# Kernel tuning notes

Hardware: AMD Instinct MI355X
Metric: run time of the kernel (lower is better)

The kernel has to match this reference:

```python
import jax, jax.numpy as jnp
import numpy as np

B, D, L, H = 256, 512, 64, 300


def setup_inputs() -> dict:
    key = jax.random.key(0)
    ks = jax.random.split(key, 16)
    s = 0.05  # weight init scale to keep activations sane through ReLU chains
    return {
        "x": jax.random.normal(ks[0], (B, D), jnp.float32),
        "eps": jax.random.normal(ks[1], (B, L), jnp.float32),
        "W": jax.random.normal(ks[2], (D, L), jnp.float32) * s,
        "enc1_w": jax.random.normal(ks[3], (H, D), jnp.float32) * s,
        "enc1_b": jax.random.normal(ks[4], (H,), jnp.float32) * s,
        "enc2_w": jax.random.normal(ks[5], (H, H), jnp.float32) * s,
        "enc2_b": jax.random.normal(ks[6], (H,), jnp.float32) * s,
        "zm_w": jax.random.normal(ks[7], (L, H), jnp.float32) * s,
        "zm_b": jax.random.normal(ks[8], (L,), jnp.float32) * s,
        "zv_w": jax.random.normal(ks[9], (L, H), jnp.float32) * s,
        "zv_b": jax.random.normal(ks[10], (L,), jnp.float32) * s,
        "gen1_w": jax.random.normal(ks[11], (H, L), jnp.float32) * s,
        "gen2_w": jax.random.normal(ks[12], (H, H), jnp.float32) * s,
        "gen2_b": jax.random.normal(ks[13], (H,), jnp.float32) * s,
        "head_w": jax.random.normal(ks[14], (D, H), jnp.float32) * s,
        "head_b": jax.random.normal(ks[15], (D,), jnp.float32) * s,
    }


def reference(x, eps, W, enc1_w, enc1_b, enc2_w, enc2_b, zm_w, zm_b,
              zv_w, zv_b, gen1_w, gen2_w, gen2_b, head_w, head_b):
    # encode: q_z = ReLU(Linear) -> ReLU(Linear)
    h = jax.nn.relu(x @ enc1_w.T + enc1_b)
    h = jax.nn.relu(h @ enc2_w.T + enc2_b)
    z_mean = h @ zm_w.T + zm_b          # [B, L]
    z_log_var = h @ zv_w.T + zv_b       # [B, L]
    # reparameterize (eps passed in for determinism)
    z = z_mean + eps * jnp.exp(0.5 * z_log_var)
    # decode: per-column masked z through shared generator + per-column head,
    # vectorized over the column axis D (mask = W rows)
    masked = z[:, None, :] * W[None, :, :]                       # [B, D, L]
    g1 = jax.nn.relu(jnp.einsum('bdl,hl->bdh', masked, gen1_w))  # [B, D, H]
    g2 = jax.nn.relu(jnp.einsum('bdh,gh->bdg', g1, gen2_w) + gen2_b)
    x_mean = jnp.einsum('bdh,dh->bd', g2, head_w) + head_b       # [B, D]
    return (x_mean, z, z_mean, z_log_var)
```

## Files before the change

### kernel.cpp

```cpp
#include <hip/hip_runtime.h>

typedef unsigned short u16;
typedef unsigned int u32;

typedef __bf16 bf16x8 __attribute__((ext_vector_type(8)));
typedef float f32x4 __attribute__((ext_vector_type(4)));

union V16 { uint4 u; bf16x8 v; u16 s[8]; __bf16 h[8]; };
union F4  { float4 v; float f[4]; };

__device__ __forceinline__ float bf2f(u16 a) {
  union { u32 u; float f; } c; c.u = ((u32)a) << 16; return c.f;
}

#define Z_OFF   131072
#define ZM_OFF  147456
#define ZLV_OFF 163840

#define B1_OFF 0
#define B2_OFF 2560
#define E1_OFF 15360
#define E2_OFF 35840
#define ZMP_OFF 48640
#define ZVP_OFF 51200
#define FRAG_TOTAL 53760
#define WB4  53760
#define XB4  57856
#define H1_4 74240
#define H2_4 84480
#define PACK_THREADS (FRAG_TOTAL + 4096 + 16384)

__device__ __forceinline__ void pack_one(const float* __restrict__ src,
                                         int t, int s, int lane,
                                         int Nsrc, int Ksrc, int rowlen,
                                         uint4* __restrict__ dst) {
  const int n = t * 16 + (lane & 15);
  const int k0 = s * 32 + ((lane >> 4) << 3);
  V16 v;
#pragma unroll
  for (int j = 0; j < 8; ++j) {
    const int k = k0 + j;
    v.h[j] = (n < Nsrc && k < Ksrc) ? (__bf16)src[n * rowlen + k] : (__bf16)0.f;
  }
  *dst = v.u;
}

__device__ __forceinline__ void cvt8(const float* __restrict__ src, uint4* __restrict__ dst) {
  F4 a, b; a.v = *(const float4*)src; b.v = *(const float4*)(src + 4);
  V16 v;
#pragma unroll
  for (int j = 0; j < 4; ++j) { v.h[j] = (__bf16)a.f[j]; v.h[4 + j] = (__bf16)b.f[j]; }
  *dst = v.u;
}

__global__ __launch_bounds__(256) void pack_kernel(
    const float* __restrict__ g1w, const float* __restrict__ g2w,
    const float* __restrict__ e1w, const float* __restrict__ e2w,
    const float* __restrict__ zmw, const float* __restrict__ zvw,
    const float* __restrict__ W,   const float* __restrict__ x,
    uint4* __restrict__ ws4) {
  const int idx = blockIdx.x * 256 + threadIdx.x;
  if (idx >= PACK_THREADS) return;
  const int lane = idx & 63;
  if (idx < B2_OFF) {
    const int f = (idx - B1_OFF) >> 6;
    pack_one(g1w, f >> 1, f & 1, lane, 300, 64, 64, ws4 + idx);
  } else if (idx < E1_OFF) {
    const int f = (idx - B2_OFF) >> 6;
    pack_one(g2w, f / 10, f % 10, lane, 300, 300, 300, ws4 + idx);
  } else if (idx < E2_OFF) {
    const int f = (idx - E1_OFF) >> 6;
    pack_one(e1w, f >> 4, f & 15, lane, 300, 512, 512, ws4 + idx);
  } else if (idx < ZMP_OFF) {
    const int f = (idx - E2_OFF) >> 6;
    pack_one(e2w, f / 10, f % 10, lane, 300, 300, 300, ws4 + idx);
  } else if (idx < ZVP_OFF) {
    const int f = (idx - ZMP_OFF) >> 6;
    pack_one(zmw, f / 10, f % 10, lane, 64, 300, 300, ws4 + idx);
  } else if (idx < FRAG_TOTAL) {
    const int f = (idx - ZVP_OFF) >> 6;
    pack_one(zvw, f / 10, f % 10, lane, 64, 300, 300, ws4 + idx);
  } else if (idx < FRAG_TOTAL + 4096) {
    const int i = idx - FRAG_TOTAL;
    cvt8(W + i * 8, ws4 + WB4 + i);
  } else {
    const int i = idx - FRAG_TOTAL - 4096;
    cvt8(x + i * 8, ws4 + XB4 + i);
  }
}

__global__ __launch_bounds__(64) void enc1_kernel(
    const uint4* __restrict__ xb, const uint4* __restrict__ e1p,
    const float* __restrict__ e1b, u16* __restrict__ h1) {
  const int wg = blockIdx.x;
  const int rt = wg / 20, nt = wg % 20;
  const int lane = threadIdx.x, q = lane >> 4, c = lane & 15;
  f32x4 acc = {0.f, 0.f, 0.f, 0.f};
  const int arow = rt * 16 + c;
#pragma unroll
  for (int s = 0; s < 16; ++s) {
    V16 a, b;
    a.u = xb[arow * 64 + s * 4 + q];
    b.u = e1p[(nt * 16 + s) * 64 + lane];
    acc = __builtin_amdgcn_mfma_f32_16x16x32_bf16(a.v, b.v, acc, 0, 0, 0);
  }
  const int col = nt * 16 + c;
  const float bias = (col < 300) ? e1b[col] : 0.f;
#pragma unroll
  for (int i = 0; i < 4; ++i) {
    const int row = rt * 16 + 4 * q + i;
    V16 t; t.h[0] = (col < 300) ? (__bf16)fmaxf(acc[i] + bias, 0.f) : (__bf16)0.f;
    h1[row * 320 + col] = t.s[0];
  }
}

__global__ __launch_bounds__(64) void enc2_kernel(
    const uint4* __restrict__ h1, const uint4* __restrict__ e2p,
    const float* __restrict__ e2b, u16* __restrict__ h2) {
  const int wg = blockIdx.x;
  const int rt = wg / 20, nt = wg % 20;
  const int lane = threadIdx.x, q = lane >> 4, c = lane & 15;
  f32x4 acc = {0.f, 0.f, 0.f, 0.f};
  const int arow = rt * 16 + c;
#pragma unroll
  for (int s = 0; s < 10; ++s) {
    V16 a, b;
    a.u = h1[arow * 40 + s * 4 + q];
    b.u = e2p[(nt * 10 + s) * 64 + lane];
    acc = __builtin_amdgcn_mfma_f32_16x16x32_bf16(a.v, b.v, acc, 0, 0, 0);
  }
  const int col = nt * 16 + c;
  const float bias = (col < 300) ? e2b[col] : 0.f;
#pragma unroll
  for (int i = 0; i < 4; ++i) {
    const int row = rt * 16 + 4 * q + i;
    V16 t; t.h[0] = (col < 300) ? (__bf16)fmaxf(acc[i] + bias, 0.f) : (__bf16)0.f;
    h2[row * 320 + col] = t.s[0];
  }
}

__global__ __launch_bounds__(64) void ench_kernel(
    const uint4* __restrict__ h2, const float* __restrict__ eps,
    const uint4* __restrict__ zmp, const float* __restrict__ zmb,
    const uint4* __restrict__ zvp, const float* __restrict__ zvb,
    float* __restrict__ out) {
  const int wg = blockIdx.x;
  const int rt = wg >> 2, t = wg & 3;
  const int lane = threadIdx.x, q = lane >> 4, c = lane & 15;
  f32x4 am = {0.f, 0.f, 0.f, 0.f}, av = {0.f, 0.f, 0.f, 0.f};
  const int arow = rt * 16 + c;
#pragma unroll
  for (int s = 0; s < 10; ++s) {
    V16 a, bm, bv;
    a.u = h2[arow * 40 + s * 4 + q];
    bm.u = zmp[(t * 10 + s) * 64 + lane];
    bv.u = zvp[(t * 10 + s) * 64 + lane];
    am = __builtin_amdgcn_mfma_f32_16x16x32_bf16(a.v, bm.v, am, 0, 0, 0);
    av = __builtin_amdgcn_mfma_f32_16x16x32_bf16(a.v, bv.v, av, 0, 0, 0);
  }
  const int col = t * 16 + c;
  const float bm = zmb[col], bv = zvb[col];
#pragma unroll
  for (int i = 0; i < 4; ++i) {
    const int gi = (rt * 16 + 4 * q + i) * 64 + col;
    const float zm = am[i] + bm;
    const float zlv = av[i] + bv;
    out[ZM_OFF + gi] = zm;
    out[ZLV_OFF + gi] = zlv;
    out[Z_OFF + gi] = zm + eps[gi] * expf(0.5f * zlv);
  }
}

__global__ __launch_bounds__(320, 4) void dec_kernel(
    const float* __restrict__ z,
    const uint4* __restrict__ Wb,
    const uint4* __restrict__ b1p,
    const uint4* __restrict__ b2p,
    const float* __restrict__ g2b,
    const float* __restrict__ hw,
    const float* __restrict__ hb,
    float* __restrict__ xout) {
  __shared__ u16 g1s[32 * 328];
  float* xredf = (float*)g1s;

  const int wg = blockIdx.x;
  const int r0 = wg << 5;
  const int bi = wg >> 4;
  const int d0 = r0 & 511;
  const int tid = threadIdx.x;
  const int u = tid >> 6;
  const int lane = tid & 63;
  const int q = lane >> 4;
  const int c = lane & 15;

  const float* zrow = z + bi * 64;

  bf16x8 bz[4][2];
#pragma unroll
  for (int kf = 0; kf < 2; ++kf) {
    F4 z0, z1;
    z0.v = *(const float4*)(zrow + kf * 32 + q * 8);
    z1.v = *(const float4*)(zrow + kf * 32 + q * 8 + 4);
#pragma unroll
    for (int tt = 0; tt < 4; ++tt) {
      V16 r; r.u = b1p[((4 * u + tt) * 2 + kf) * 64 + lane];
      V16 m;
#pragma unroll
      for (int j = 0; j < 4; ++j) {
        m.h[j]     = (__bf16)(bf2f(r.s[j])     * z0.f[j]);
        m.h[4 + j] = (__bf16)(bf2f(r.s[4 + j]) * z1.f[j]);
      }
      bz[tt][kf] = m.v;
    }
  }
#pragma unroll
  for (int rt = 0; rt < 2; ++rt) {
    const int rowA = rt * 16 + c;
    V16 af0, af1;
    af0.u = Wb[(d0 + rowA) * 8 + q];
    af1.u = Wb[(d0 + rowA) * 8 + 4 + q];
    f32x4 acc[4];
#pragma unroll
    for (int tt = 0; tt < 4; ++tt) acc[tt] = {0.f, 0.f, 0.f, 0.f};
#pragma unroll
    for (int tt = 0; tt < 4; ++tt) {
      acc[tt] = __builtin_amdgcn_mfma_f32_16x16x32_bf16(af0.v, bz[tt][0], acc[tt], 0, 0, 0);
      acc[tt] = __builtin_amdgcn_mfma_f32_16x16x32_bf16(af1.v, bz[tt][1], acc[tt], 0, 0, 0);
    }
    const int rwb = rt * 16 + 4 * q;
#pragma unroll
    for (int tt = 0; tt < 4; ++tt) {
      const int colb = (4 * u + tt) * 16 + c;
#pragma unroll
      for (int i = 0; i < 4; ++i) {
        V16 t; t.h[0] = (__bf16)fmaxf(acc[tt][i], 0.f);
        g1s[(rwb + i) * 328 + colb] = t.s[0];
      }
    }
  }
  __syncthreads();

  f32x4 a3[4][2];
#pragma unroll
  for (int tt = 0; tt < 4; ++tt)
#pragma unroll
    for (int rt = 0; rt < 2; ++rt) a3[tt][rt] = {0.f, 0.f, 0.f, 0.f};
  for (int s = 0; s < 10; ++s) {
    V16 b[4];
#pragma unroll
    for (int tt = 0; tt < 4; ++tt) b[tt].u = b2p[((4 * u + tt) * 10 + s) * 64 + lane];
#pragma unroll
    for (int rt = 0; rt < 2; ++rt) {
      V16 a; a.u = *(const uint4*)&g1s[(rt * 16 + c) * 328 + s * 32 + q * 8];
#pragma unroll
      for (int tt = 0; tt < 4; ++tt)
        a3[tt][rt] = __builtin_amdgcn_mfma_f32_16x16x32_bf16(a.v, b[tt].v, a3[tt][rt], 0, 0, 0);
    }
  }
  float xacc[2][4];
#pragma unroll
  for (int rt = 0; rt < 2; ++rt)
#pragma unroll
    for (int i = 0; i < 4; ++i) xacc[rt][i] = 0.f;
#pragma unroll
  for (int tt = 0; tt < 4; ++tt) {
    const int col = (4 * u + tt) * 16 + c;
    const bool inb = (col < 300);
    const float bias = inb ? g2b[col] : 0.f;
#pragma unroll
    for (int rt = 0; rt < 2; ++rt)
#pragma unroll
      for (int i = 0; i < 4; ++i) {
        const float g2v = fmaxf(a3[tt][rt][i] + bias, 0.f);
        const float h = inb ? hw[(d0 + rt * 16 + 4 * q + i) * 300 + col] : 0.f;
        xacc[rt][i] += g2v * h;
      }
  }
#pragma unroll
  for (int rt = 0; rt < 2; ++rt)
#pragma unroll
    for (int i = 0; i < 4; ++i) {
      float t = xacc[rt][i];
      t += __shfl_xor(t, 1);
      t += __shfl_xor(t, 2);
      t += __shfl_xor(t, 4);
      t += __shfl_xor(t, 8);
      xacc[rt][i] = t;
    }
  __syncthreads();
  if (c < 4) {
#pragma unroll
    for (int rt = 0; rt < 2; ++rt) {
      float t = xacc[rt][0];
      t = (c == 1) ? xacc[rt][1] : t;
      t = (c == 2) ? xacc[rt][2] : t;
      t = (c == 3) ? xacc[rt][3] : t;
      xredf[u * 32 + rt * 16 + 4 * q + c] = t;
    }
  }
  __syncthreads();
  if (tid < 32) {
    float t = hb[d0 + tid];
#pragma unroll
    for (int uu = 0; uu < 5; ++uu) t += xredf[uu * 32 + tid];
    xout[r0 + tid] = t;
  }
}

extern "C" void kernel_launch(void* const* d_in, const int* in_sizes, int n_in,
                              void* d_out, int out_size, void* d_ws, size_t ws_size,
                              hipStream_t stream) {
  const float* x   = (const float*)d_in[0];
  const float* eps = (const float*)d_in[1];
  const float* W   = (const float*)d_in[2];
  const float* e1w = (const float*)d_in[3];
  const float* e1b = (const float*)d_in[4];
  const float* e2w = (const float*)d_in[5];
  const float* e2b = (const float*)d_in[6];
  const float* zmw = (const float*)d_in[7];
  const float* zmb = (const float*)d_in[8];
  const float* zvw = (const float*)d_in[9];
  const float* zvb = (const float*)d_in[10];
  const float* g1w = (const float*)d_in[11];
  const float* g2w = (const float*)d_in[12];
  const float* g2b = (const float*)d_in[13];
  const float* hw  = (const float*)d_in[14];
  const float* hb  = (const float*)d_in[15];
  float* out = (float*)d_out;
  uint4* ws4 = (uint4*)d_ws;

  pack_kernel<<<(PACK_THREADS + 255) / 256, 256, 0, stream>>>(
      g1w, g2w, e1w, e2w, zmw, zvw, W, x, ws4);
  enc1_kernel<<<320, 64, 0, stream>>>(ws4 + XB4, ws4 + E1_OFF, e1b, (u16*)(ws4 + H1_4));
  enc2_kernel<<<320, 64, 0, stream>>>(ws4 + H1_4, ws4 + E2_OFF, e2b, (u16*)(ws4 + H2_4));
  ench_kernel<<<64, 64, 0, stream>>>(ws4 + H2_4, eps,
                                     ws4 + ZMP_OFF, zmb, ws4 + ZVP_OFF, zvb, out);
  dec_kernel<<<4096, 320, 0, stream>>>(out + Z_OFF, ws4 + WB4,
                                       ws4 + B1_OFF, ws4 + B2_OFF,
                                       g2b, hw, hb, out);
}
```

Baseline: 164.3 us.

## Split decoder work across ten waves and apply z mask to W operand

```diff
diff --git a/kernel.cpp b/kernel.cpp
--- a/kernel.cpp
+++ b/kernel.cpp
@@ -28,7 +28,7 @@
 #define XB4  57856
 #define H1_4 74240
 #define H2_4 84480
-#define PACK_THREADS (FRAG_TOTAL + 4096 + 16384)
+#define PACK_THREADS 74240
 
 __device__ __forceinline__ void pack_one(const float* __restrict__ src,
                                          int t, int s, int lane,
@@ -63,7 +63,7 @@
   if (idx >= PACK_THREADS) return;
   const int lane = idx & 63;
   if (idx < B2_OFF) {
-    const int f = (idx - B1_OFF) >> 6;
+    const int f = idx >> 6;
     pack_one(g1w, f >> 1, f & 1, lane, 300, 64, 64, ws4 + idx);
   } else if (idx < E1_OFF) {
     const int f = (idx - B2_OFF) >> 6;
@@ -80,11 +80,11 @@
   } else if (idx < FRAG_TOTAL) {
     const int f = (idx - ZVP_OFF) >> 6;
     pack_one(zvw, f / 10, f % 10, lane, 64, 300, 300, ws4 + idx);
-  } else if (idx < FRAG_TOTAL + 4096) {
-    const int i = idx - FRAG_TOTAL;
+  } else if (idx < XB4) {
+    const int i = idx - WB4;
     cvt8(W + i * 8, ws4 + WB4 + i);
   } else {
-    const int i = idx - FRAG_TOTAL - 4096;
+    const int i = idx - XB4;
     cvt8(x + i * 8, ws4 + XB4 + i);
   }
 }
@@ -171,7 +171,7 @@
   }
 }
 
-__global__ __launch_bounds__(320, 4) void dec_kernel(
+__global__ __launch_bounds__(640, 5) void dec_kernel(
     const float* __restrict__ z,
     const uint4* __restrict__ Wb,
     const uint4* __restrict__ b1p,
@@ -195,66 +195,78 @@
 
   const float* zrow = z + bi * 64;
 
-  bf16x8 bz[4][2];
-#pragma unroll
-  for (int kf = 0; kf < 2; ++kf) {
-    F4 z0, z1;
-    z0.v = *(const float4*)(zrow + kf * 32 + q * 8);
-    z1.v = *(const float4*)(zrow + kf * 32 + q * 8 + 4);
-#pragma unroll
-    for (int tt = 0; tt < 4; ++tt) {
-      V16 r; r.u = b1p[((4 * u + tt) * 2 + kf) * 64 + lane];
-      V16 m;
-#pragma unroll
-      for (int j = 0; j < 4; ++j) {
-        m.h[j]     = (__bf16)(bf2f(r.s[j])     * z0.f[j]);
-        m.h[4 + j] = (__bf16)(bf2f(r.s[4 + j]) * z1.f[j]);
+  F4 z0a, z0b, z1a, z1b;
+  z0a.v = *(const float4*)(zrow + q * 8);
+  z0b.v = *(const float4*)(zrow + q * 8 + 4);
+  z1a.v = *(const float4*)(zrow + 32 + q * 8);
+  z1b.v = *(const float4*)(zrow + 32 + q * 8 + 4);
+
+  bf16x8 af[2][2];
+#pragma unroll
+  for (int rt = 0; rt < 2; ++rt) {
+    V16 w0, w1, m;
+    w0.u = Wb[(d0 + rt * 16 + c) * 8 + q];
+    w1.u = Wb[(d0 + rt * 16 + c) * 8 + 4 + q];
+#pragma unroll
+    for (int j = 0; j < 4; ++j) {
+      m.h[j]     = (__bf16)(bf2f(w0.s[j])     * z0a.f[j]);
+      m.h[4 + j] = (__bf16)(bf2f(w0.s[4 + j]) * z0b.f[j]);
+    }
+    af[rt][0] = m.v;
+#pragma unroll
+    for (int j = 0; j < 4; ++j) {
+      m.h[j]     = (__bf16)(bf2f(w1.s[j])     * z1a.f[j]);
+      m.h[4 + j] = (__bf16)(bf2f(w1.s[4 + j]) * z1b.f[j]);
+    }
+    af[rt][1] = m.v;
+  }
+  {
+    f32x4 acc[2][2];
+#pragma unroll
+    for (int ttl = 0; ttl < 2; ++ttl)
+#pragma unroll
+      for (int rt = 0; rt < 2; ++rt) acc[ttl][rt] = {0.f, 0.f, 0.f, 0.f};
+#pragma unroll
+    for (int ttl = 0; ttl < 2; ++ttl) {
+      V16 b0, b1;
+      b0.u = b1p[((2 * u + ttl) * 2 + 0) * 64 + lane];
+      b1.u = b1p[((2 * u + ttl) * 2 + 1) * 64 + lane];
+#pragma unroll
+      for (int rt = 0; rt < 2; ++rt) {
+        acc[ttl][rt] = __builtin_amdgcn_mfma_f32_16x16x32_bf16(af[rt][0], b0.v, acc[ttl][rt], 0, 0, 0);
+        acc[ttl][rt] = __builtin_amdgcn_mfma_f32_16x16x32_bf16(af[rt][1], b1.v, acc[ttl][rt], 0, 0, 0);
       }
-      bz[tt][kf] = m.v;
-    }
-  }
-#pragma unroll
-  for (int rt = 0; rt < 2; ++rt) {
-    const int rowA = rt * 16 + c;
-    V16 af0, af1;
-    af0.u = Wb[(d0 + rowA) * 8 + q];
-    af1.u = Wb[(d0 + rowA) * 8 + 4 + q];
-    f32x4 acc[4];
-#pragma unroll
-    for (int tt = 0; tt < 4; ++tt) acc[tt] = {0.f, 0.f, 0.f, 0.f};
-#pragma unroll
-    for (int tt = 0; tt < 4; ++tt) {
-      acc[tt] = __builtin_amdgcn_mfma_f32_16x16x32_bf16(af0.v, bz[tt][0], acc[tt], 0, 0, 0);
-      acc[tt] = __builtin_amdgcn_mfma_f32_16x16x32_bf16(af1.v, bz[tt][1], acc[tt], 0, 0, 0);
-    }
-    const int rwb = rt * 16 + 4 * q;
-#pragma unroll
-    for (int tt = 0; tt < 4; ++tt) {
-      const int colb = (4 * u + tt) * 16 + c;
-#pragma unroll
-      for (int i = 0; i < 4; ++i) {
-        V16 t; t.h[0] = (__bf16)fmaxf(acc[tt][i], 0.f);
-        g1s[(rwb + i) * 328 + colb] = t.s[0];
+    }
+#pragma unroll
+    for (int ttl = 0; ttl < 2; ++ttl) {
+      const int colb = (2 * u + ttl) * 16 + c;
+#pragma unroll
+      for (int rt = 0; rt < 2; ++rt) {
+        const int rwb = rt * 16 + 4 * q;
+#pragma unroll
+        for (int i = 0; i < 4; ++i) {
+          V16 t; t.h[0] = (__bf16)fmaxf(acc[ttl][rt][i], 0.f);
+          g1s[(rwb + i) * 328 + colb] = t.s[0];
+        }
       }
     }
   }
   __syncthreads();
 
-  f32x4 a3[4][2];
-#pragma unroll
-  for (int tt = 0; tt < 4; ++tt)
-#pragma unroll
-    for (int rt = 0; rt < 2; ++rt) a3[tt][rt] = {0.f, 0.f, 0.f, 0.f};
+  f32x4 a3[2][2];
+#pragma unroll
+  for (int ttl = 0; ttl < 2; ++ttl)
+#pragma unroll
+    for (int rt = 0; rt < 2; ++rt) a3[ttl][rt] = {0.f, 0.f, 0.f, 0.f};
   for (int s = 0; s < 10; ++s) {
-    V16 b[4];
-#pragma unroll
-    for (int tt = 0; tt < 4; ++tt) b[tt].u = b2p[((4 * u + tt) * 10 + s) * 64 + lane];
+    V16 b0, b1;
+    b0.u = b2p[((2 * u + 0) * 10 + s) * 64 + lane];
+    b1.u = b2p[((2 * u + 1) * 10 + s) * 64 + lane];
 #pragma unroll
     for (int rt = 0; rt < 2; ++rt) {
       V16 a; a.u = *(const uint4*)&g1s[(rt * 16 + c) * 328 + s * 32 + q * 8];
-#pragma unroll
-      for (int tt = 0; tt < 4; ++tt)
-        a3[tt][rt] = __builtin_amdgcn_mfma_f32_16x16x32_bf16(a.v, b[tt].v, a3[tt][rt], 0, 0, 0);
+      a3[0][rt] = __builtin_amdgcn_mfma_f32_16x16x32_bf16(a.v, b0.v, a3[0][rt], 0, 0, 0);
+      a3[1][rt] = __builtin_amdgcn_mfma_f32_16x16x32_bf16(a.v, b1.v, a3[1][rt], 0, 0, 0);
     }
   }
   float xacc[2][4];
@@ -263,15 +275,15 @@
 #pragma unroll
     for (int i = 0; i < 4; ++i) xacc[rt][i] = 0.f;
 #pragma unroll
-  for (int tt = 0; tt < 4; ++tt) {
-    const int col = (4 * u + tt) * 16 + c;
+  for (int ttl = 0; ttl < 2; ++ttl) {
+    const int col = (2 * u + ttl) * 16 + c;
     const bool inb = (col < 300);
     const float bias = inb ? g2b[col] : 0.f;
 #pragma unroll
     for (int rt = 0; rt < 2; ++rt)
 #pragma unroll
       for (int i = 0; i < 4; ++i) {
-        const float g2v = fmaxf(a3[tt][rt][i] + bias, 0.f);
+        const float g2v = fmaxf(a3[ttl][rt][i] + bias, 0.f);
         const float h = inb ? hw[(d0 + rt * 16 + 4 * q + i) * 300 + col] : 0.f;
         xacc[rt][i] += g2v * h;
       }
@@ -302,7 +314,7 @@
   if (tid < 32) {
     float t = hb[d0 + tid];
 #pragma unroll
-    for (int uu = 0; uu < 5; ++uu) t += xredf[uu * 32 + tid];
+    for (int uu = 0; uu < 10; ++uu) t += xredf[uu * 32 + tid];
     xout[r0 + tid] = t;
   }
 }
@@ -335,7 +347,7 @@
   enc2_kernel<<<320, 64, 0, stream>>>(ws4 + H1_4, ws4 + E2_OFF, e2b, (u16*)(ws4 + H2_4));
   ench_kernel<<<64, 64, 0, stream>>>(ws4 + H2_4, eps,
                                      ws4 + ZMP_OFF, zmb, ws4 + ZVP_OFF, zvb, out);
-  dec_kernel<<<4096, 320, 0, stream>>>(out + Z_OFF, ws4 + WB4,
+  dec_kernel<<<4096, 640, 0, stream>>>(out + Z_OFF, ws4 + WB4,
                                        ws4 + B1_OFF, ws4 + B2_OFF,
                                        g2b, hw, hb, out);
 }
```

Measured after the change: 180.4 us. +9.8%, slower.
